# Optimization experiments

Measured on AMD Instinct MI355X. Metric: run time of the kernel, lower is better.

Reference implementation:

```python
import jax, jax.numpy as jnp
import numpy as np

EPS_TINY = np.float32(np.finfo(np.float32).tiny)  # torch clamp min in continuous_topk


def layernorm(x, gamma, beta, eps=1e-6):
    mu = jnp.mean(x, axis=-1, keepdims=True)
    var = jnp.mean((x - mu) ** 2, axis=-1, keepdims=True)
    return (x - mu) * jax.lax.rsqrt(var + eps) * gamma + beta


def continuous_topk(w, k, t=0.1):
    """Iterative differentiable top-k with hard straight-through, as in the torch code.
    w: (B, N) logits. Returns khot: (B, k, N)."""
    n = w.shape[-1]

    def step(carry, _):
        logits, onehot = carry
        # khot_mask = clamp(1 - onehot, min=EPS); logits accumulate log-mask in place
        logits = logits + jnp.log(jnp.maximum(1.0 - onehot, EPS_TINY))
        soft = jax.nn.softmax(logits / t, axis=-1)
        hard = jax.nn.one_hot(jnp.argmax(soft, axis=-1), n, dtype=soft.dtype)
        st = hard - jax.lax.stop_gradient(soft) + soft  # straight-through
        return (logits, st), st

    (_, _), khot = jax.lax.scan(step, (w, jnp.zeros_like(w)), None, length=k)
    return jnp.transpose(khot, (1, 0, 2))  # (k,B,N) -> (B,k,N)


def setup_inputs():
    key = jax.random.key(0)
    ks = jax.random.split(key, 8)
    B, N, C, COUT = 8, 2048, 256, 256
    s = 0.02
    return {
        "xyzs": jax.random.normal(ks[0], (B, N, 3), jnp.float32),
        "features": jax.random.normal(ks[1], (B, C, N), jnp.float32),
        "ln_gamma": jnp.ones((C,), jnp.float32),
        "ln_beta": jnp.zeros((C,), jnp.float32),
        "Wu1": jax.random.normal(ks[2], (C, C), jnp.float32) * s,
        "bu1": jnp.zeros((C,), jnp.float32),
        "Wu2": jax.random.normal(ks[3], (C, COUT), jnp.float32) * s,
        "bu2": jnp.zeros((COUT,), jnp.float32),
        "Wd1": jax.random.normal(ks[4], (C, C), jnp.float32) * s,
        "bd1": jnp.zeros((C,), jnp.float32),
        "Wd2": jax.random.normal(ks[5], (C, 1), jnp.float32) * s,
        "bd2": jnp.zeros((1,), jnp.float32),
        "out_num_points": 1024,
    }


def reference(xyzs, features, ln_gamma, ln_beta, Wu1, bu1, Wu2, bu2, Wd1, bd1, Wd2, bd2, out_num_points):
    # eval mode: dropout inactive, gumbel_keys skipped (self.training False)
    f = jnp.transpose(features, (0, 2, 1))           # (B, N, C)
    f = layernorm(f, ln_gamma, ln_beta)
    new_f = jnp.maximum(f @ Wu1 + bu1, 0.0) @ Wu2 + bu2   # (B, N, COUT)
    w = (jnp.maximum(f @ Wd1 + bd1, 0.0) @ Wd2 + bd2)[:, :, 0]  # (B, N)
    khot = continuous_topk(w, out_num_points, t=0.1)  # (B, K, N)
    xyzs_out = khot @ xyzs                            # (B, K, 3)
    feats = jnp.einsum('bkn,bnc->bkc', khot, new_f)   # (B, K, COUT)
    indices = jnp.argmax(khot, axis=2)                # (B, K)
    return xyzs_out, jnp.transpose(feats, (0, 2, 1)), indices
```

## Files before the change

### kernel.cpp

```cpp
#include <hip/hip_runtime.h>

#define B_DIM 8
#define N_DIM 2048
#define C_DIM 256
#define K_SEL 1024

typedef __attribute__((ext_vector_type(8))) short short8;
typedef __attribute__((ext_vector_type(4))) float f32x4;

__device__ __forceinline__ unsigned int bf16rne(float x) {
  unsigned int u = __float_as_uint(x);
  return (u + 0x7fffu + ((u >> 16) & 1u)) >> 16;
}

__global__ __launch_bounds__(256) void ln_lds(const float* __restrict__ feat,
    const float* __restrict__ gamma, const float* __restrict__ beta,
    float* __restrict__ fbuf) {
  __shared__ float tile[256 * 64];
  __shared__ float murs[128];
  const int t = threadIdx.x;
  const int m0 = blockIdx.x << 6;
  const int b = m0 >> 11, n0 = m0 & 2047;

  const int cg = t >> 4, nl4 = (t & 15) << 2;
  for (int pass = 0; pass < 16; ++pass) {
    const int c = (pass << 4) + cg;
    const float4 v = *(const float4*)(feat + (((long)((b << 8) + c)) << 11) + n0 + nl4);
    const int sw = c & 31;
    float* row = tile + (c << 6);
    row[(nl4 + 0) ^ sw] = v.x; row[(nl4 + 1) ^ sw] = v.y;
    row[(nl4 + 2) ^ sw] = v.z; row[(nl4 + 3) ^ sw] = v.w;
  }
  __syncthreads();

  if (t < 64) {
    float acc = tile[t];
    for (int c = 1; c < 256; ++c) acc = __fadd_rn(acc, tile[(c << 6) + (t ^ (c & 31))]);
    const float mu = __fdiv_rn(acc, 256.0f);

    float pw[2];
#pragma unroll
    for (int blk = 0; blk < 2; ++blk) {
      const int c0 = blk << 7;
      float r8[8];
#pragma unroll
      for (int j = 0; j < 8; ++j) {
        float d = __fsub_rn(tile[((c0 + j) << 6) + (t ^ ((c0 + j) & 31))], mu);
        r8[j] = __fmul_rn(d, d);
      }
      for (int i = 8; i < 128; i += 8) {
#pragma unroll
        for (int j = 0; j < 8; ++j) {
          const int c = c0 + i + j;
          float d = __fsub_rn(tile[(c << 6) + (t ^ (c & 31))], mu);
          r8[j] = __fadd_rn(r8[j], __fmul_rn(d, d));
        }
      }
      pw[blk] = __fadd_rn(__fadd_rn(__fadd_rn(r8[0], r8[1]), __fadd_rn(r8[2], r8[3])),
                          __fadd_rn(__fadd_rn(r8[4], r8[5]), __fadd_rn(r8[6], r8[7])));
    }
    const float var = __fdiv_rn(__fadd_rn(pw[0], pw[1]), 256.0f);
    const float rs = __fdiv_rn(1.0f, __fsqrt_rn(__fadd_rn(var, 1e-6f)));
    murs[t] = mu;
    murs[64 + t] = rs;
  }
  __syncthreads();

  const int tc = t & 63, rg = t >> 6;
  const int c0 = tc << 2;
  const float4 g4 = *(const float4*)(gamma + c0);
  const float4 b4 = *(const float4*)(beta + c0);
  const float ga[4] = {g4.x, g4.y, g4.z, g4.w};
  const float be[4] = {b4.x, b4.y, b4.z, b4.w};
  for (int rr = 0; rr < 16; ++rr) {
    const int r = (rg << 4) + rr;
    const float mu_r = murs[r];
    const float rs_r = murs[64 + r];
    float4 o;
    float ov[4];
#pragma unroll
    for (int q = 0; q < 4; ++q) {
      const int c = c0 + q;
      const float x = tile[(c << 6) + (r ^ (c & 31))];
      ov[q] = __fadd_rn(__fmul_rn(__fmul_rn(__fsub_rn(x, mu_r), rs_r), ga[q]), be[q]);
    }
    o.x = ov[0]; o.y = ov[1]; o.z = ov[2]; o.w = ov[3];
    *(float4*)(fbuf + (((long)(m0 + r)) << 8) + c0) = o;
  }
}

__global__ void __launch_bounds__(512) wgemm_w(
    const float* __restrict__ A, const float* __restrict__ Wd1,
    const float* __restrict__ bd1, const float* __restrict__ Wd2,
    const float* __restrict__ bd2, float* __restrict__ wkey) {
  __shared__ __align__(16) char smem[65536];
  float (*As)[68] = (float (*)[68])smem;
  float (*Bs)[260] = (float (*)[260])(smem + 4352);
  float* H = (float*)smem;

  const int t = threadIdx.x;
  const int m0 = blockIdx.x << 6;
  const int rowT = t >> 6, colT = t & 63;
  const int ar = t >> 2, ak = (t & 3) << 2;
  const int bk = t >> 5, bc = (t & 31) << 3;
  const long arow = ((long)(m0 + ar)) << 8;
  float acc[8][4] = {};

  for (int k0 = 0; k0 < 256; k0 += 16) {
    if (t < 256) {
      const float4 av = *(const float4*)(A + arow + k0 + ak);
      As[ak + 0][ar] = av.x; As[ak + 1][ar] = av.y;
      As[ak + 2][ar] = av.z; As[ak + 3][ar] = av.w;
    }
    const float* brow = Wd1 + (((k0 + bk) << 8) + bc);
    *(float4*)&Bs[bk][bc] = *(const float4*)brow;
    *(float4*)&Bs[bk][bc + 4] = *(const float4*)(brow + 4);
    __syncthreads();
#pragma unroll
    for (int kk = 0; kk < 16; ++kk) {
      const float4 a0 = *(const float4*)&As[kk][rowT << 3];
      const float4 a1 = *(const float4*)&As[kk][(rowT << 3) + 4];
      const float4 b = *(const float4*)&Bs[kk][colT << 2];
      const float aa[8] = {a0.x, a0.y, a0.z, a0.w, a1.x, a1.y, a1.z, a1.w};
      const float bbv[4] = {b.x, b.y, b.z, b.w};
#pragma unroll
      for (int i = 0; i < 8; ++i)
#pragma unroll
        for (int j = 0; j < 4; ++j)
          acc[i][j] = __fmaf_rn(aa[i], bbv[j], acc[i][j]);
    }
    __syncthreads();
  }

  const float4 bd = *(const float4*)(bd1 + (colT << 2));
  const float ba[4] = {bd.x, bd.y, bd.z, bd.w};
#pragma unroll
  for (int i = 0; i < 8; ++i) {
    const int m = (rowT << 3) + i;
#pragma unroll
    for (int j = 0; j < 4; ++j) {
      const int c = (colT << 2) + j;
      H[(c << 6) + (m ^ ((c >> 2) & 31))] = fmaxf(__fadd_rn(acc[i][j], ba[j]), 0.0f);
    }
  }
  __syncthreads();

  if (t < 64) {
    float wa = 0.0f;
    for (int c = 0; c < 256; ++c)
      wa = __fmaf_rn(H[(c << 6) + (t ^ ((c >> 2) & 31))], Wd2[c], wa);
    const float w = __fadd_rn(wa, bd2[0]);
    wkey[m0 + t] = __fdiv_rn(w, 0.1f);
  }
}

__global__ void __launch_bounds__(1024) topk_kernel(
    const float* __restrict__ wv, const float* __restrict__ xyzs,
    int* __restrict__ idx_out, float* __restrict__ out_xyz,
    float* __restrict__ out_idx) {
  __shared__ unsigned long long vals[2048];
  const int b = blockIdx.x, t = threadIdx.x;
#pragma unroll
  for (int h = 0; h < 2; ++h) {
    const int i = (h << 10) + t;
    const unsigned int u = __float_as_uint(wv[(b << 11) + i]);
    const unsigned int up = ((int)u < 0) ? ~u : (u | 0x80000000u);
    vals[i] = (((unsigned long long)(~up)) << 32) | (unsigned int)i;
  }
  __syncthreads();
  for (int k = 2; k <= 2048; k <<= 1) {
    for (int j = k >> 1; j > 0; j >>= 1) {
      for (int half = 0; half < 2; ++half) {
        const int i = (half << 10) | t;
        const int ixj = i ^ j;
        if (ixj > i) {
          const unsigned long long vi = vals[i], vj = vals[ixj];
          const bool up = ((i & k) == 0);
          if ((vi > vj) == up) { vals[i] = vj; vals[ixj] = vi; }
        }
      }
      __syncthreads();
    }
  }
  const int sel = (int)(vals[t] & 0xffffffffu);
  idx_out[(b << 10) + t] = sel;
  out_idx[(b << 10) + t] = (float)sel;
  const long o = ((long)((b << 10) + t)) * 3;
  const long s3 = ((long)((b << 11) + sel)) * 3;
  out_xyz[o] = xyzs[s3]; out_xyz[o + 1] = xyzs[s3 + 1]; out_xyz[o + 2] = xyzs[s3 + 2];
}

__global__ __launch_bounds__(256) void prep_w2(const float* __restrict__ W1,
    const float* __restrict__ W2, unsigned short* __restrict__ P1,
    unsigned short* __restrict__ P2) {
  const int g = blockIdx.x;
  const float* W = (g < 8) ? W1 : W2;
  unsigned short* P = (g < 8) ? P1 : P2;
  const int kc = g & 7, n = threadIdx.x;
  unsigned int packed[16];
#pragma unroll
  for (int i = 0; i < 16; ++i) {
    const float a = W[(((kc << 5) + 2 * i) << 8) + n];
    const float bq = W[(((kc << 5) + 2 * i + 1) << 8) + n];
    packed[i] = bf16rne(a) | (bf16rne(bq) << 16);
  }
  uint4* dst = (uint4*)(P + (((kc << 8) + n) << 5));
#pragma unroll
  for (int q = 0; q < 4; ++q)
    dst[q] = make_uint4(packed[4 * q], packed[4 * q + 1], packed[4 * q + 2], packed[4 * q + 3]);
}

#define APITCH 264
#define BPITCH 40
__global__ void __launch_bounds__(256) up_mfma(
    const float* __restrict__ fbuf, const int* __restrict__ idxm,
    const unsigned short* __restrict__ Wu1P, const float* __restrict__ bu1,
    const unsigned short* __restrict__ Wu2P, const float* __restrict__ bu2,
    float* __restrict__ out_feat) {
  __shared__ __align__(16) char smem[64 * APITCH * 2 + 256 * BPITCH * 2 + 2048];
  unsigned short* As = (unsigned short*)smem;
  unsigned short* Bs = (unsigned short*)(smem + 64 * APITCH * 2);
  float* bias1 = (float*)(smem + 64 * APITCH * 2 + 256 * BPITCH * 2);
  float* bias2 = bias1 + 256;
  float* T = (float*)(smem + 64 * APITCH * 2);

  const int t = threadIdx.x;
  const int m0 = blockIdx.x << 6;
  const int quad = (t >> 4) & 3, ln = t & 15, w = t >> 6;

  bias1[t] = bu1[t];
  bias2[t] = bu2[t];

  {
    const int r = t & 63, cseg = t >> 6;
    const int m = m0 + r;
    const long srow = (long)(((m >> 10) << 11) + idxm[m]) << 8;
    const float* src = fbuf + srow + (cseg << 6);
    unsigned short* dst = As + r * APITCH + (cseg << 6);
#pragma unroll
    for (int u = 0; u < 16; ++u) {
      const float4 v = *(const float4*)(src + (u << 2));
      const unsigned int lo = bf16rne(v.x) | (bf16rne(v.y) << 16);
      const unsigned int hi = bf16rne(v.z) | (bf16rne(v.w) << 16);
      *(uint2*)(dst + (u << 2)) = make_uint2(lo, hi);
    }
  }

  f32x4 acc[16];
#pragma unroll
  for (int i = 0; i < 16; ++i) acc[i] = (f32x4){0.f, 0.f, 0.f, 0.f};

  for (int kc = 0; kc < 8; ++kc) {
    __syncthreads();
    const uint4* sb = (const uint4*)(Wu1P + (((kc << 8) + t) << 5));
    uint4* db = (uint4*)(Bs + t * BPITCH);
    db[0] = sb[0]; db[1] = sb[1]; db[2] = sb[2]; db[3] = sb[3];
    __syncthreads();
    const short8 a = *(const short8*)(As + ((w << 4) + ln) * APITCH + (kc << 5) + (quad << 3));
#pragma unroll
    for (int nt = 0; nt < 16; ++nt) {
      const short8 b = *(const short8*)(Bs + ((nt << 4) + ln) * BPITCH + (quad << 3));
      acc[nt] = __builtin_amdgcn_mfma_f32_16x16x32_bf16(a, b, acc[nt], 0, 0, 0);
    }
  }

  __syncthreads();
  unsigned short* Hs = As;
#pragma unroll
  for (int nt = 0; nt < 16; ++nt) {
    const int c = (nt << 4) + ln;
    const float bb = bias1[c];
#pragma unroll
    for (int rr = 0; rr < 4; ++rr) {
      const float h = fmaxf(acc[nt][rr] + bb, 0.0f);
      Hs[((w << 4) + (quad << 2) + rr) * APITCH + c] = (unsigned short)bf16rne(h);
    }
  }
#pragma unroll
  for (int i = 0; i < 16; ++i) acc[i] = (f32x4){0.f, 0.f, 0.f, 0.f};

  for (int kc = 0; kc < 8; ++kc) {
    __syncthreads();
    const uint4* sb = (const uint4*)(Wu2P + (((kc << 8) + t) << 5));
    uint4* db = (uint4*)(Bs + t * BPITCH);
    db[0] = sb[0]; db[1] = sb[1]; db[2] = sb[2]; db[3] = sb[3];
    __syncthreads();
    const short8 a = *(const short8*)(Hs + ((w << 4) + ln) * APITCH + (kc << 5) + (quad << 3));
#pragma unroll
    for (int nt = 0; nt < 16; ++nt) {
      const short8 b = *(const short8*)(Bs + ((nt << 4) + ln) * BPITCH + (quad << 3));
      acc[nt] = __builtin_amdgcn_mfma_f32_16x16x32_bf16(a, b, acc[nt], 0, 0, 0);
    }
  }

  const int bb = m0 >> 10, kbase = m0 & 1023;
  for (int ci = 0; ci < 4; ++ci) {
    __syncthreads();
#pragma unroll
    for (int q = 0; q < 4; ++q) {
      const int nt = (ci << 2) + q;
      const int cloc = (q << 4) + ln;
      const float b2 = bias2[(nt << 4) + ln];
#pragma unroll
      for (int rr = 0; rr < 4; ++rr)
        T[cloc * 66 + ((w << 4) + (quad << 2) + rr)] = acc[nt][rr] + b2;
    }
    __syncthreads();
#pragma unroll
    for (int p = 0; p < 16; ++p) {
      const int cl = (p << 2) + (t >> 6);
      const int m = t & 63;
      out_feat[((long)((bb << 8) + (ci << 6) + cl) << 10) + kbase + m] = T[cl * 66 + m];
    }
  }
}

extern "C" void kernel_launch(void* const* d_in, const int* in_sizes, int n_in,
                              void* d_out, int out_size, void* d_ws, size_t ws_size,
                              hipStream_t stream) {
  const float* xyzs     = (const float*)d_in[0];
  const float* features = (const float*)d_in[1];
  const float* ln_gamma = (const float*)d_in[2];
  const float* ln_beta  = (const float*)d_in[3];
  const float* Wu1      = (const float*)d_in[4];
  const float* bu1      = (const float*)d_in[5];
  const float* Wu2      = (const float*)d_in[6];
  const float* bu2      = (const float*)d_in[7];
  const float* Wd1      = (const float*)d_in[8];
  const float* bd1      = (const float*)d_in[9];
  const float* Wd2      = (const float*)d_in[10];
  const float* bd2      = (const float*)d_in[11];

  char* ws = (char*)d_ws;
  float* fbuf = (float*)ws;
  unsigned short* Wu1P = (unsigned short*)(ws + 33554432);
  unsigned short* Wu2P = (unsigned short*)(ws + 33685504);
  float* wv   = (float*)(ws + 50331648);
  int*   idx  = (int*)(ws + 50397184);

  float* out_xyz  = (float*)d_out;
  float* out_feat = out_xyz + 24576;
  float* out_idx  = out_feat + 2097152;

  prep_w2<<<16, 256, 0, stream>>>(Wu1, Wu2, Wu1P, Wu2P);
  ln_lds<<<256, 256, 0, stream>>>(features, ln_gamma, ln_beta, fbuf);
  wgemm_w<<<256, 512, 0, stream>>>(fbuf, Wd1, bd1, Wd2, bd2, wv);
  topk_kernel<<<8, 1024, 0, stream>>>(wv, xyzs, idx, out_xyz, out_idx);
  up_mfma<<<128, 256, 0, stream>>>(fbuf, idx, Wu1P, bu1, Wu2P, bu2, out_feat);
}
```

Before: 187.7 us.

## Broadcast A operand via readlane from registers instead of LDS staging

```diff
diff --git a/kernel.cpp b/kernel.cpp
--- a/kernel.cpp
+++ b/kernel.cpp
@@ -94,42 +94,51 @@
     const float* __restrict__ bd1, const float* __restrict__ Wd2,
     const float* __restrict__ bd2, float* __restrict__ wkey) {
   __shared__ __align__(16) char smem[65536];
-  float (*As)[68] = (float (*)[68])smem;
-  float (*Bs)[260] = (float (*)[260])(smem + 4352);
+  float (*Bs)[260] = (float (*)[260])smem;
   float* H = (float*)smem;
 
   const int t = threadIdx.x;
   const int m0 = blockIdx.x << 6;
   const int rowT = t >> 6, colT = t & 63;
-  const int ar = t >> 2, ak = (t & 3) << 2;
-  const int bk = t >> 5, bc = (t & 31) << 3;
-  const long arow = ((long)(m0 + ar)) << 8;
+  const int lane = t & 63;
+  const int bk = t >> 5, bl4 = (t & 31) << 2;
+  const float* aload = A + ((long)(m0 + (rowT << 3) + (lane & 7)) << 8) + ((lane >> 3) << 2);
+
   float acc[8][4] = {};
 
-  for (int k0 = 0; k0 < 256; k0 += 16) {
-    if (t < 256) {
-      const float4 av = *(const float4*)(A + arow + k0 + ak);
-      As[ak + 0][ar] = av.x; As[ak + 1][ar] = av.y;
-      As[ak + 2][ar] = av.z; As[ak + 3][ar] = av.w;
-    }
-    const float* brow = Wd1 + (((k0 + bk) << 8) + bc);
-    *(float4*)&Bs[bk][bc] = *(const float4*)brow;
-    *(float4*)&Bs[bk][bc + 4] = *(const float4*)(brow + 4);
-    __syncthreads();
-#pragma unroll
-    for (int kk = 0; kk < 16; ++kk) {
-      const float4 a0 = *(const float4*)&As[kk][rowT << 3];
-      const float4 a1 = *(const float4*)&As[kk][(rowT << 3) + 4];
-      const float4 b = *(const float4*)&Bs[kk][colT << 2];
-      const float aa[8] = {a0.x, a0.y, a0.z, a0.w, a1.x, a1.y, a1.z, a1.w};
-      const float bbv[4] = {b.x, b.y, b.z, b.w};
-#pragma unroll
-      for (int i = 0; i < 8; ++i)
-#pragma unroll
-        for (int j = 0; j < 4; ++j)
-          acc[i][j] = __fmaf_rn(aa[i], bbv[j], acc[i][j]);
-    }
-    __syncthreads();
+  float4 ac = *(const float4*)(aload);
+
+  for (int ch = 0; ch < 8; ++ch) {
+    const int chn = (ch < 7) ? ch + 1 : 7;
+    const float4 an = *(const float4*)(aload + (chn << 5));
+#pragma unroll
+    for (int h = 0; h < 2; ++h) {
+      const int k0 = (ch << 5) + (h << 4);
+      {
+        const float* brow = Wd1 + ((k0 + bk) << 8);
+        *(float4*)&Bs[bk][bl4]       = *(const float4*)(brow + bl4);
+        *(float4*)&Bs[bk][bl4 + 128] = *(const float4*)(brow + bl4 + 128);
+      }
+      __syncthreads();
+#pragma unroll
+      for (int kk = 0; kk < 16; ++kk) {
+        const int kkl = (h << 4) + kk;
+        const float4 b = *(const float4*)&Bs[kk][colT << 2];
+        const float bbv[4] = {b.x, b.y, b.z, b.w};
+        const float av_src = (kkl & 3) == 0 ? ac.x : (kkl & 3) == 1 ? ac.y
+                           : (kkl & 3) == 2 ? ac.z : ac.w;
+#pragma unroll
+        for (int i = 0; i < 8; ++i) {
+          const float aval = __uint_as_float(__builtin_amdgcn_readlane(
+              __float_as_uint(av_src), ((kkl >> 2) << 3) + i));
+#pragma unroll
+          for (int j = 0; j < 4; ++j)
+            acc[i][j] = __fmaf_rn(aval, bbv[j], acc[i][j]);
+        }
+      }
+      __syncthreads();
+    }
+    ac = an;
   }
 
   const float4 bd = *(const float4*)(bd1 + (colT << 2));
```

After: 187.6 us. No clear change (-0.1%).

## Fuse layernorm into the score GEMM kernel, reading normalized rows from LDS

Applied to the files above, without the earlier changes.

```diff
diff --git a/kernel.cpp b/kernel.cpp
--- a/kernel.cpp
+++ b/kernel.cpp
@@ -13,18 +13,30 @@
   return (u + 0x7fffu + ((u >> 16) & 1u)) >> 16;
 }
 
-__global__ __launch_bounds__(256) void ln_lds(const float* __restrict__ feat,
-    const float* __restrict__ gamma, const float* __restrict__ beta,
-    float* __restrict__ fbuf) {
-  __shared__ float tile[256 * 64];
+__global__ void __launch_bounds__(512) ln_wgemm(
+    const float* __restrict__ feat, const float* __restrict__ gamma,
+    const float* __restrict__ beta, float* __restrict__ fbuf,
+    const float* __restrict__ Wd1, const float* __restrict__ bd1,
+    const float* __restrict__ Wd2, const float* __restrict__ bd2,
+    float* __restrict__ wkey) {
+  __shared__ __align__(16) float tile[256 * 64];
+  __shared__ __align__(16) char smem2[4352 + 16640];
   __shared__ float murs[128];
+  __shared__ float gb[512];
+  float (*As)[68] = (float (*)[68])smem2;
+  float (*Bs)[260] = (float (*)[260])(smem2 + 4352);
+  float* H = tile;
+
   const int t = threadIdx.x;
   const int m0 = blockIdx.x << 6;
   const int b = m0 >> 11, n0 = m0 & 2047;
 
+  if (t < 256) gb[t] = gamma[t];
+  else gb[t] = beta[t - 256];
+
   const int cg = t >> 4, nl4 = (t & 15) << 2;
-  for (int pass = 0; pass < 16; ++pass) {
-    const int c = (pass << 4) + cg;
+  for (int pass = 0; pass < 8; ++pass) {
+    const int c = (pass << 5) + cg;
     const float4 v = *(const float4*)(feat + (((long)((b << 8) + c)) << 11) + n0 + nl4);
     const int sw = c & 31;
     float* row = tile + (c << 6);
@@ -66,51 +78,45 @@
   }
   __syncthreads();
 
-  const int tc = t & 63, rg = t >> 6;
-  const int c0 = tc << 2;
-  const float4 g4 = *(const float4*)(gamma + c0);
-  const float4 b4 = *(const float4*)(beta + c0);
-  const float ga[4] = {g4.x, g4.y, g4.z, g4.w};
-  const float be[4] = {b4.x, b4.y, b4.z, b4.w};
-  for (int rr = 0; rr < 16; ++rr) {
-    const int r = (rg << 4) + rr;
-    const float mu_r = murs[r];
-    const float rs_r = murs[64 + r];
-    float4 o;
-    float ov[4];
-#pragma unroll
-    for (int q = 0; q < 4; ++q) {
-      const int c = c0 + q;
-      const float x = tile[(c << 6) + (r ^ (c & 31))];
-      ov[q] = __fadd_rn(__fmul_rn(__fmul_rn(__fsub_rn(x, mu_r), rs_r), ga[q]), be[q]);
-    }
-    o.x = ov[0]; o.y = ov[1]; o.z = ov[2]; o.w = ov[3];
-    *(float4*)(fbuf + (((long)(m0 + r)) << 8) + c0) = o;
-  }
-}
-
-__global__ void __launch_bounds__(512) wgemm_w(
-    const float* __restrict__ A, const float* __restrict__ Wd1,
-    const float* __restrict__ bd1, const float* __restrict__ Wd2,
-    const float* __restrict__ bd2, float* __restrict__ wkey) {
-  __shared__ __align__(16) char smem[65536];
-  float (*As)[68] = (float (*)[68])smem;
-  float (*Bs)[260] = (float (*)[260])(smem + 4352);
-  float* H = (float*)smem;
-
-  const int t = threadIdx.x;
-  const int m0 = blockIdx.x << 6;
+  {
+    const int tc = t & 63, rg = t >> 6;
+    const int c0 = tc << 2;
+    const float4 g4 = *(const float4*)(gamma + c0);
+    const float4 b4 = *(const float4*)(beta + c0);
+    const float ga[4] = {g4.x, g4.y, g4.z, g4.w};
+    const float be[4] = {b4.x, b4.y, b4.z, b4.w};
+    for (int rr = 0; rr < 8; ++rr) {
+      const int r = (rg << 3) + rr;
+      const float mu_r = murs[r];
+      const float rs_r = murs[64 + r];
+      float ov[4];
+#pragma unroll
+      for (int q = 0; q < 4; ++q) {
+        const int c = c0 + q;
+        const float x = tile[(c << 6) + (r ^ (c & 31))];
+        ov[q] = __fadd_rn(__fmul_rn(__fmul_rn(__fsub_rn(x, mu_r), rs_r), ga[q]), be[q]);
+      }
+      float4 o; o.x = ov[0]; o.y = ov[1]; o.z = ov[2]; o.w = ov[3];
+      *(float4*)(fbuf + (((long)(m0 + r)) << 8) + c0) = o;
+    }
+  }
+
   const int rowT = t >> 6, colT = t & 63;
   const int ar = t >> 2, ak = (t & 3) << 2;
   const int bk = t >> 5, bc = (t & 31) << 3;
-  const long arow = ((long)(m0 + ar)) << 8;
+  float mu_a = 0.0f, rs_a = 0.0f;
+  if (t < 256) { mu_a = murs[ar]; rs_a = murs[64 + ar]; }
   float acc[8][4] = {};
 
   for (int k0 = 0; k0 < 256; k0 += 16) {
     if (t < 256) {
-      const float4 av = *(const float4*)(A + arow + k0 + ak);
-      As[ak + 0][ar] = av.x; As[ak + 1][ar] = av.y;
-      As[ak + 2][ar] = av.z; As[ak + 3][ar] = av.w;
+#pragma unroll
+      for (int q = 0; q < 4; ++q) {
+        const int c = k0 + ak + q;
+        const float x = tile[(c << 6) + (ar ^ (c & 31))];
+        As[ak + q][ar] = __fadd_rn(
+            __fmul_rn(__fmul_rn(__fsub_rn(x, mu_a), rs_a), gb[c]), gb[256 + c]);
+      }
     }
     const float* brow = Wd1 + (((k0 + bk) << 8) + bc);
     *(float4*)&Bs[bk][bc] = *(const float4*)brow;
@@ -120,9 +126,9 @@
     for (int kk = 0; kk < 16; ++kk) {
       const float4 a0 = *(const float4*)&As[kk][rowT << 3];
       const float4 a1 = *(const float4*)&As[kk][(rowT << 3) + 4];
-      const float4 b = *(const float4*)&Bs[kk][colT << 2];
+      const float4 bq = *(const float4*)&Bs[kk][colT << 2];
       const float aa[8] = {a0.x, a0.y, a0.z, a0.w, a1.x, a1.y, a1.z, a1.w};
-      const float bbv[4] = {b.x, b.y, b.z, b.w};
+      const float bbv[4] = {bq.x, bq.y, bq.z, bq.w};
 #pragma unroll
       for (int i = 0; i < 8; ++i)
 #pragma unroll
@@ -343,8 +349,8 @@
   float* out_idx  = out_feat + 2097152;
 
   prep_w2<<<16, 256, 0, stream>>>(Wu1, Wu2, Wu1P, Wu2P);
-  ln_lds<<<256, 256, 0, stream>>>(features, ln_gamma, ln_beta, fbuf);
-  wgemm_w<<<256, 512, 0, stream>>>(fbuf, Wd1, bd1, Wd2, bd2, wv);
+  ln_wgemm<<<256, 512, 0, stream>>>(features, ln_gamma, ln_beta, fbuf,
+                                    Wd1, bd1, Wd2, bd2, wv);
   topk_kernel<<<8, 1024, 0, stream>>>(wv, xyzs, idx, out_xyz, out_idx);
   up_mfma<<<128, 256, 0, stream>>>(fbuf, idx, Wu1P, bu1, Wu2P, bu2, out_feat);
 }
```

New measurement: 184.2 us. Within noise of the previous version (-1.9%).
